# Kernel tuning notes

Hardware: AMD Instinct MI355X
Metric: run time of the kernel (lower is better)

The kernel has to match this reference:

```python
import jax, jax.numpy as jnp
import numpy as np

B, L, E, H = 4, 2048, 1024, 16
DK = E // H


def setup_inputs() -> dict:
    key = jax.random.key(0)
    k1, k2, k3 = jax.random.split(key, 3)
    x = jax.random.normal(k1, (B, L, E), dtype=jnp.float32)
    # torch Linear weights are [out, in]; xavier-ish scaling
    w_qkv = jax.random.normal(k2, (3 * E, E), dtype=jnp.float32) * (2.0 / (E + 3 * E)) ** 0.5
    wo = jax.random.normal(k3, (E, E), dtype=jnp.float32) * (1.0 / E) ** 0.5
    # causal mask: scores filled with -inf where mask == 0
    mask = jnp.tril(jnp.ones((L, L), dtype=bool))
    return {"x": x, "mask": mask, "w_qkv": w_qkv, "wo": wo}


def reference(x, mask, w_qkv, wo):
    b, l, e = x.shape
    # qkv projection: Linear with weight [3E, E] -> x @ W^T
    qkv = x @ w_qkv.T                              # [b, l, 3E]
    qkv = qkv.reshape(b, l, 3, H, DK)              # (three h d) split
    q = jnp.transpose(qkv[:, :, 0], (0, 2, 1, 3))  # [b, h, l, d]
    k = jnp.transpose(qkv[:, :, 1], (0, 2, 1, 3))
    v = jnp.transpose(qkv[:, :, 2], (0, 2, 1, 3))
    scores = jnp.einsum('bhld,bhmd->bhlm', q, k) / np.sqrt(DK)  # [b, h, l, l]
    scores = jnp.where(mask, scores, -jnp.inf)
    attn = jax.nn.softmax(scores, axis=-1)
    out = jnp.einsum('bhlm,bhmd->bhld', attn, v)   # [b, h, l, d]
    out = jnp.transpose(out, (0, 2, 1, 3)).reshape(b, l, e)  # b l (h d)
    return out @ wo.T
```

## Files before the change

kernel.cpp:

```cpp
#include <hip/hip_runtime.h>
#include <stdint.h>


typedef __bf16 bf16;
typedef __bf16 bf16x4 __attribute__((ext_vector_type(4)));
typedef __bf16 bf16x8 __attribute__((ext_vector_type(8)));
typedef float floatx4 __attribute__((ext_vector_type(4)));
typedef short s16x4 __attribute__((ext_vector_type(4)));

#define MFMA32(a, b, c) __builtin_amdgcn_mfma_f32_16x16x32_bf16(a, b, c, 0, 0, 0)
#define MFMA16(a, b, c) __builtin_amdgcn_mfma_f32_16x16x16bf16_1k(a, b, c, 0, 0, 0)

typedef const __attribute__((address_space(1))) uint32_t* gas_t;
typedef __attribute__((address_space(3))) uint32_t* las_t;

__device__ __forceinline__ void async16(void* lds, const void* g) {
  __builtin_amdgcn_global_load_lds((gas_t)g, (las_t)lds, 16, 0, 0);
}

__global__ void cvt_all(const float4* __restrict__ x, const float4* __restrict__ wq,
                        const float4* __restrict__ wo, bf16x4* __restrict__ xb,
                        bf16x4* __restrict__ wqb, bf16x4* __restrict__ wob) {
  const int NX = 2097152, NQ = 786432;
  int i = blockIdx.x * blockDim.x + threadIdx.x;
  float4 v;
  bf16x4* dst;
  int j;
  if (i < NX) { j = i; v = x[j]; dst = xb; }
  else if (i < NX + NQ) { j = i - NX; v = wq[j]; dst = wqb; }
  else { j = i - NX - NQ; v = wo[j]; dst = wob; }
  bf16x4 o;
  o[0] = (bf16)v.x; o[1] = (bf16)v.y; o[2] = (bf16)v.z; o[3] = (bf16)v.w;
  dst[j] = o;
}

__global__ __launch_bounds__(512, 2) void gemm_qkv(
    const bf16* __restrict__ A, const bf16* __restrict__ B,
    bf16* __restrict__ Qb, bf16* __restrict__ Kb, bf16* __restrict__ Vt) {
  __shared__ __align__(16) bf16 lds[2 * 24576];
  const int tid = threadIdx.x;
  const int wave = tid >> 6, lane = tid & 63;
  const int wr = wave >> 1, wc = wave & 1;
  const int l15 = lane & 15, quad = lane >> 4;

  const int bid = blockIdx.x;
  const int xcd = bid & 7, j = bid >> 3;
  const int mt_i = xcd * 4 + (j / 24);
  const int nt_i = j % 24;
  const int m0 = mt_i * 256, n0 = nt_i * 128;

  const int s_r = lane >> 3, s_c = lane & 7;

  auto unit = [&](bf16* dst, const bf16* src) {
#pragma unroll
    for (int i = 0; i < 2; ++i) {
      int g = wave * 2 + i;
      int row = g * 8 + s_r;
      async16(&dst[g * 512], src + (size_t)row * 1024 + ((s_c ^ (row & 7)) << 3));
    }
  };

  const bf16* Asrc = A + (size_t)m0 * 1024;
  const bf16* Bsrc = B + (size_t)n0 * 1024;

  auto rdA = [&](const bf16* cb, int mt, int kk) -> bf16x8 {
    int row = wr * 64 + mt * 16 + l15;
    return *(const bf16x8*)&cb[row * 64 + ((((kk << 2) | quad) ^ (l15 & 7)) << 3)];
  };
  auto rdB = [&](const bf16* cb, int nt, int kk) -> bf16x8 {
    int row = wc * 64 + nt * 16 + l15;
    return *(const bf16x8*)&cb[16384 + row * 64 +
                               ((((kk << 2) | quad) ^ (l15 & 7)) << 3)];
  };

  floatx4 acc[4][4] = {};

  unit(lds,         Asrc);
  unit(lds + 8192,  Asrc + (size_t)128 * 1024);
  unit(lds + 16384, Bsrc);

  auto body = [&](int t, bf16* cb, bf16* nb) {
    const int k1 = (t + 1) << 6;
    const bool pre = (t + 1) < 16;
    if (pre) {
      unit(nb, Asrc + k1);
      asm volatile("s_waitcnt vmcnt(2)" ::: "memory");
    } else {
      asm volatile("s_waitcnt vmcnt(0)" ::: "memory");
    }
    __builtin_amdgcn_s_barrier();
    asm volatile("" ::: "memory");
    bf16x8 bfr[4][2];
#pragma unroll
    for (int nt = 0; nt < 4; ++nt)
#pragma unroll
      for (int kk = 0; kk < 2; ++kk) bfr[nt][kk] = rdB(cb, nt, kk);
    bf16x8 af[2][2];
#pragma unroll
    for (int mt = 0; mt < 2; ++mt)
#pragma unroll
      for (int kk = 0; kk < 2; ++kk) af[mt][kk] = rdA(cb, mt, kk);
    __builtin_amdgcn_s_setprio(1);
#pragma unroll
    for (int mt = 0; mt < 2; ++mt)
#pragma unroll
      for (int nt = 0; nt < 4; ++nt)
#pragma unroll
        for (int kk = 0; kk < 2; ++kk)
          acc[mt][nt] = MFMA32(af[mt][kk], bfr[nt][kk], acc[mt][nt]);
    __builtin_amdgcn_s_setprio(0);
    if (pre) unit(nb + 8192, Asrc + (size_t)128 * 1024 + k1);
#pragma unroll
    for (int mt = 0; mt < 2; ++mt)
#pragma unroll
      for (int kk = 0; kk < 2; ++kk) af[mt][kk] = rdA(cb, mt + 2, kk);
    if (pre) unit(nb + 16384, Bsrc + k1);
    __builtin_amdgcn_s_setprio(1);
#pragma unroll
    for (int mt = 0; mt < 2; ++mt)
#pragma unroll
      for (int nt = 0; nt < 4; ++nt)
#pragma unroll
        for (int kk = 0; kk < 2; ++kk)
          acc[mt + 2][nt] = MFMA32(af[mt][kk], bfr[nt][kk], acc[mt + 2][nt]);
    __builtin_amdgcn_s_setprio(0);
    __builtin_amdgcn_s_barrier();
    asm volatile("" ::: "memory");
  };

  for (int tt = 0; tt < 8; ++tt) {
    body(2 * tt,     lds,         lds + 24576);
    body(2 * tt + 1, lds + 24576, lds);
  }

  if (n0 < 2048) {
    bf16* outp = (n0 < 1024) ? Qb : Kb;
    const int hd0 = n0 & 1023;
#pragma unroll
    for (int mt = 0; mt < 4; ++mt)
#pragma unroll
      for (int nt = 0; nt < 4; ++nt)
#pragma unroll
        for (int r = 0; r < 4; ++r) {
          int gm = m0 + wr * 64 + mt * 16 + quad * 4 + r;
          int gh = hd0 + wc * 64 + nt * 16 + l15;
          outp[(size_t)gm * 1024 + gh] = (bf16)acc[mt][nt][r];
        }
    return;
  }
  const int hd0 = n0 - 2048;
  const int bb = m0 >> 11, l_base = m0 & 2047;
#pragma unroll
  for (int mt = 0; mt < 4; ++mt)
#pragma unroll
    for (int nt = 0; nt < 4; ++nt) {
      int hd_l = wc * 64 + nt * 16 + l15;
      int l_l = wr * 64 + mt * 16 + quad * 4;
      bf16x4 tv;
#pragma unroll
      for (int r = 0; r < 4; ++r) tv[r] = (bf16)acc[mt][nt][r];
      *(bf16x4*)&lds[hd_l * 264 + l_l] = tv;
    }
  __syncthreads();
  const int rr = tid >> 5, cc = tid & 31;
#pragma unroll
  for (int it = 0; it < 8; ++it) {
    int row = it * 16 + rr;
    bf16x8 v = *(const bf16x8*)&lds[row * 264 + cc * 8];
    int hd = hd0 + row;
    *(bf16x8*)&Vt[((((size_t)bb * 16 + (hd >> 6)) * 64 + (hd & 63)) << 11) +
                  l_base + cc * 8] = v;
  }
}

__global__ __launch_bounds__(256) void gemm2_64(
    const bf16* __restrict__ A, const bf16* __restrict__ B,
    float* __restrict__ Cf, int M, int N, int K) {
  __shared__ __align__(16) bf16 As[64 * 32];
  __shared__ __align__(16) bf16 Bs[128 * 32];
  const int tid = threadIdx.x;
  const int wave = tid >> 6, lane = tid & 63;
  const int row0 = blockIdx.y * 64, col0 = blockIdx.x * 128;
  const int l15 = lane & 15, quad = lane >> 4;
  const int srow = lane >> 2, scol = (lane & 3) * 8;

  floatx4 acc[4][2] = {};

  for (int k0 = 0; k0 < K; k0 += 32) {
#pragma unroll
    for (int i = 0; i < 3; ++i) {
      int c = wave * 3 + i;
      if (c < 4)
        async16(&As[c * 512], A + (size_t)(row0 + c * 16 + srow) * K + k0 + scol);
      else
        async16(&Bs[(c - 4) * 512],
                B + (size_t)(col0 + (c - 4) * 16 + srow) * K + k0 + scol);
    }
    __syncthreads();
    bf16x8 af[4], bfr[2];
#pragma unroll
    for (int t = 0; t < 4; ++t)
      af[t] = *(const bf16x8*)&As[(t * 16 + l15) * 32 + quad * 8];
#pragma unroll
    for (int t = 0; t < 2; ++t)
      bfr[t] = *(const bf16x8*)&Bs[(wave * 32 + t * 16 + l15) * 32 + quad * 8];
#pragma unroll
    for (int mt = 0; mt < 4; ++mt)
#pragma unroll
      for (int nt = 0; nt < 2; ++nt)
        acc[mt][nt] = MFMA32(af[mt], bfr[nt], acc[mt][nt]);
    __syncthreads();
  }

#pragma unroll
  for (int mt = 0; mt < 4; ++mt)
#pragma unroll
    for (int nt = 0; nt < 2; ++nt)
#pragma unroll
      for (int r = 0; r < 4; ++r) {
        int gr = row0 + mt * 16 + quad * 4 + r;
        int gc = col0 + wave * 32 + nt * 16 + l15;
        Cf[(size_t)gr * N + gc] = acc[mt][nt][r];
      }
}

__global__ __launch_bounds__(256, 2) void flash_attn(
    const bf16* __restrict__ Qb, const bf16* __restrict__ Kb,
    const bf16* __restrict__ Vt, bf16* __restrict__ Ob) {
  const int bid0 = blockIdx.x;
  const int xcd = bid0 & 7, jj = bid0 >> 3;
  const int bh = xcd * 8 + (jj & 7);
  const int pr = jj >> 3;
  const int b = bh >> 4, h = bh & 15;
  const int tid = threadIdx.x;
  const int wave = tid >> 6, lane = tid & 63;
  const int l15 = lane & 15, quad = lane >> 4;

  const int qA = pr, qB = 31 - pr;

  __shared__ __align__(16) bf16 Ks2[2 * 64 * 64];
  __shared__ __align__(16) bf16 Vs2[2 * 64 * 64];

  const size_t x_base = (size_t)b * 2048 * 1024 + (size_t)h * 64;
  const size_t vt_base = (size_t)bh * 64 * 2048;

  const int k_lr = lane >> 3, k_c = lane & 7;

  auto stage = [&](int kt, int bufsel) {
    bf16* Kd = Ks2 + bufsel * 4096;
    bf16* Vd = Vs2 + bufsel * 4096;
#pragma unroll
    for (int i = 0; i < 2; ++i) {
      int o8 = wave * 2 + i;
      int row = o8 * 8 + k_lr;
      int sw = (k_c ^ (row & 7)) << 3;
      async16(&Kd[o8 * 512],
              Kb + x_base + (size_t)(kt * 64 + row) * 1024 + sw);
      async16(&Vd[o8 * 512],
              Vt + vt_base + (size_t)row * 2048 + kt * 64 + sw);
    }
  };

  auto load_q = [&](int q64, bf16x8* qf) {
#pragma unroll
    for (int ks = 0; ks < 2; ++ks) {
      const bf16* p = Qb + x_base +
          (size_t)(q64 * 64 + wave * 16 + l15) * 1024 + ks * 32 + quad * 8;
      bf16x8 v = *(const bf16x8*)p;
#pragma unroll
      for (int j = 0; j < 8; ++j) v[j] = (bf16)((float)v[j] * 0.18033688f);
      qf[ks] = v;
    }
  };

  stage(0, 0);

  bf16x8 qfA[2], qfB[2];
  load_q(qA, qfA);
  load_q(qB, qfB);

  floatx4 oA[4] = {}, oB[4] = {};
  float lA = 0.f, lB = 0.f;

  auto process = [&](const bf16x8* qf, floatx4* o, float& l_run,
                     int kt, int q64, bool diag, const bf16* Ks, const bf16* Vs) {
    floatx4 s[4] = {};
    __builtin_amdgcn_s_setprio(1);
#pragma unroll
    for (int nt = 0; nt < 4; ++nt) {
      int krow = nt * 16 + l15;
#pragma unroll
      for (int ks = 0; ks < 2; ++ks) {
        bf16x8 kf = *(const bf16x8*)&Ks[krow * 64 +
            ((((ks << 2) | quad) ^ (l15 & 7)) << 3)];
        s[nt] = MFMA32(kf, qf[ks], s[nt]);
      }
    }
    __builtin_amdgcn_s_setprio(0);
    if (diag) {
      int q_g = q64 * 64 + wave * 16 + l15;
#pragma unroll
      for (int nt = 0; nt < 4; ++nt)
#pragma unroll
        for (int r = 0; r < 4; ++r)
          if (kt * 64 + nt * 16 + quad * 4 + r > q_g) s[nt][r] = -__builtin_inff();
    }
    float ls = 0.f;
#pragma unroll
    for (int nt = 0; nt < 4; ++nt)
#pragma unroll
      for (int r = 0; r < 4; ++r) {
        float p = exp2f(s[nt][r]);
        s[nt][r] = p;
        ls += p;
      }
    l_run += ls;

    __builtin_amdgcn_s_setprio(1);
#pragma unroll
    for (int kb = 0; kb < 4; ++kb) {
      bf16x4 pb;
#pragma unroll
      for (int r = 0; r < 4; ++r) pb[r] = (bf16)s[kb][r];
      s16x4 pf = __builtin_bit_cast(s16x4, pb);
#pragma unroll
      for (int dt = 0; dt < 4; ++dt) {
        s16x4 vf = *(const s16x4*)&Vs[(dt * 16 + l15) * 64 +
            (((((kb << 1) | (quad >> 1)) ^ (l15 & 7))) << 3) + ((quad & 1) << 2)];
        o[dt] = MFMA16(vf, pf, o[dt]);
      }
    }
    __builtin_amdgcn_s_setprio(0);
  };

  __syncthreads();

  int cur = 0;
  for (int kt = 0; kt <= qB; ++kt) {
    if (kt < qB) stage(kt + 1, cur ^ 1);
    const bf16* Kc = Ks2 + cur * 4096;
    const bf16* Vc = Vs2 + cur * 4096;
    process(qfB, oB, lB, kt, qB, kt == qB, Kc, Vc);
    if (kt <= qA) process(qfA, oA, lA, kt, qA, kt == qA, Kc, Vc);
    __syncthreads();
    cur ^= 1;
  }

  auto store_o = [&](const floatx4* o, float l_run, int q64) {
    float lf = l_run;
    lf += __shfl_xor(lf, 16);
    lf += __shfl_xor(lf, 32);
    float inv = 1.0f / lf;
    size_t rowoff = x_base + (size_t)(q64 * 64 + wave * 16 + l15) * 1024;
#pragma unroll
    for (int dt = 0; dt < 4; ++dt) {
      bf16x4 ob;
#pragma unroll
      for (int r = 0; r < 4; ++r) ob[r] = (bf16)(o[dt][r] * inv);
      *(bf16x4*)(Ob + rowoff + dt * 16 + quad * 4) = ob;
    }
  };
  store_o(oA, lA, qA);
  store_o(oB, lB, qB);
}

extern "C" void kernel_launch(void* const* d_in, const int* in_sizes, int n_in,
                              void* d_out, int out_size, void* d_ws, size_t ws_size,
                              hipStream_t stream) {
  const float* x     = (const float*)d_in[0];
  const float* w_qkv = (const float*)d_in[2];
  const float* wo    = (const float*)d_in[3];
  float* out = (float*)d_out;

  char* ws = (char*)d_ws;
  bf16* xb  = (bf16*)(ws);
  bf16* wqb = (bf16*)(ws + (16u << 20));
  bf16* wob = (bf16*)(ws + (22u << 20));
  bf16* Qb  = (bf16*)(ws + (24u << 20));
  bf16* Kb  = (bf16*)(ws + (40u << 20));
  bf16* Vt  = (bf16*)(ws + (56u << 20));
  bf16* Ab  = (bf16*)(ws);

  cvt_all<<<12288, 256, 0, stream>>>((const float4*)x, (const float4*)w_qkv,
                                     (const float4*)wo, (bf16x4*)xb,
                                     (bf16x4*)wqb, (bf16x4*)wob);

  gemm_qkv<<<768, 512, 0, stream>>>(xb, wqb, Qb, Kb, Vt);
  flash_attn<<<1024, 256, 0, stream>>>(Qb, Kb, Vt, Ab);
  gemm2_64<<<dim3(8, 128), 256, 0, stream>>>(Ab, wob, out, 8192, 1024, 1024);
}
```

Baseline: 266.5 us.

## Double-buffer output projection GEMM with swizzled LDS and XCD-aware tile mapping

Rewrites the output-projection GEMM to double-buffer its LDS tiles, so the async global-to-LDS load for the next K slice overlaps the MFMAs on the current one, and it drops one barrier per iteration. An XOR swizzle on the 16-byte column chunks is meant to cut LDS bank conflicts on fragment reads. Blocks are remapped to a 1D grid so that neighbouring row tiles stay on the same XCD for L2 reuse, and wave priority is raised around the MFMAs. Dimensions are now hardcoded, so the kernel only handles this shape, and it uses twice the LDS.

Result: faster. 251.4 us (-5.7%).

```diff
diff --git a/kernel.cpp b/kernel.cpp
--- a/kernel.cpp
+++ b/kernel.cpp
@@ -175,41 +175,61 @@
 
 __global__ __launch_bounds__(256) void gemm2_64(
     const bf16* __restrict__ A, const bf16* __restrict__ B,
-    float* __restrict__ Cf, int M, int N, int K) {
-  __shared__ __align__(16) bf16 As[64 * 32];
-  __shared__ __align__(16) bf16 Bs[128 * 32];
+    float* __restrict__ Cf) {
+  __shared__ __align__(16) bf16 lds[2 * 6144];
   const int tid = threadIdx.x;
   const int wave = tid >> 6, lane = tid & 63;
-  const int row0 = blockIdx.y * 64, col0 = blockIdx.x * 128;
   const int l15 = lane & 15, quad = lane >> 4;
-  const int srow = lane >> 2, scol = (lane & 3) * 8;
-
-  floatx4 acc[4][2] = {};
-
-  for (int k0 = 0; k0 < K; k0 += 32) {
+  const int bid = blockIdx.x;
+  const int xcd = bid & 7, j = bid >> 3;
+  const int row0 = (xcd * 16 + (j >> 3)) * 64;
+  const int col0 = (j & 7) * 128;
+  const int s_r = lane >> 2, s_c = lane & 3;
+
+  auto stage = [&](int k0, bf16* buf) {
 #pragma unroll
     for (int i = 0; i < 3; ++i) {
       int c = wave * 3 + i;
-      if (c < 4)
-        async16(&As[c * 512], A + (size_t)(row0 + c * 16 + srow) * K + k0 + scol);
-      else
-        async16(&Bs[(c - 4) * 512],
-                B + (size_t)(col0 + (c - 4) * 16 + srow) * K + k0 + scol);
-    }
-    __syncthreads();
+      if (c < 4) {
+        int row = c * 16 + s_r;
+        async16(&buf[c * 512],
+                A + (size_t)(row0 + row) * 1024 + k0 + ((s_c ^ (row & 3)) << 3));
+      } else {
+        int row = (c - 4) * 16 + s_r;
+        async16(&buf[c * 512],
+                B + (size_t)(col0 + row) * 1024 + k0 + ((s_c ^ (row & 3)) << 3));
+      }
+    }
+  };
+
+  floatx4 acc[4][2] = {};
+  stage(0, lds);
+  __syncthreads();
+
+  int cur = 0;
+  for (int t = 0; t < 32; ++t) {
+    bf16* cb = lds + cur * 6144;
+    if (t < 31) stage((t + 1) << 5, lds + (cur ^ 1) * 6144);
     bf16x8 af[4], bfr[2];
 #pragma unroll
-    for (int t = 0; t < 4; ++t)
-      af[t] = *(const bf16x8*)&As[(t * 16 + l15) * 32 + quad * 8];
-#pragma unroll
-    for (int t = 0; t < 2; ++t)
-      bfr[t] = *(const bf16x8*)&Bs[(wave * 32 + t * 16 + l15) * 32 + quad * 8];
+    for (int mt = 0; mt < 4; ++mt) {
+      int row = mt * 16 + l15;
+      af[mt] = *(const bf16x8*)&cb[row * 32 + ((quad ^ (l15 & 3)) << 3)];
+    }
+#pragma unroll
+    for (int nt = 0; nt < 2; ++nt) {
+      int row = wave * 32 + nt * 16 + l15;
+      bfr[nt] = *(const bf16x8*)&cb[2048 + row * 32 + ((quad ^ (l15 & 3)) << 3)];
+    }
+    __builtin_amdgcn_s_setprio(1);
 #pragma unroll
     for (int mt = 0; mt < 4; ++mt)
 #pragma unroll
       for (int nt = 0; nt < 2; ++nt)
         acc[mt][nt] = MFMA32(af[mt], bfr[nt], acc[mt][nt]);
+    __builtin_amdgcn_s_setprio(0);
     __syncthreads();
+    cur ^= 1;
   }
 
 #pragma unroll
@@ -220,7 +240,7 @@
       for (int r = 0; r < 4; ++r) {
         int gr = row0 + mt * 16 + quad * 4 + r;
         int gc = col0 + wave * 32 + nt * 16 + l15;
-        Cf[(size_t)gr * N + gc] = acc[mt][nt][r];
+        Cf[(size_t)gr * 1024 + gc] = acc[mt][nt][r];
       }
 }
 
@@ -387,5 +407,5 @@
 
   gemm_qkv<<<768, 512, 0, stream>>>(xb, wqb, Qb, Kb, Vt);
   flash_attn<<<1024, 256, 0, stream>>>(Qb, Kb, Vt, Ab);
-  gemm2_64<<<dim3(8, 128), 256, 0, stream>>>(Ab, wob, out, 8192, 1024, 1024);
-}
+  gemm2_64<<<1024, 256, 0, stream>>>(Ab, wob, out);
+}
```

## Rewrite output projection GEMM with 256x128 tiles, double-buffered swizzled LDS

Applied to the files above, without the earlier changes.

Replaces the small 64x128 output-projection GEMM with a 512-thread kernel that computes 256x128 tiles using a BK=64 double-buffered LDS pipeline. Global-to-LDS loads for the next K step are interleaved with MFMA work, LDS uses an XOR swizzle to avoid bank conflicts, and blocks are remapped so tiles sharing rows stay on the same XCD. This aims to cut redundant global reads and hide memory latency in the final GEMM. In exchange it uses more LDS and registers per block, and the dimensions are hardcoded.

Measured after the change: 250.0 us. 6.2% less time.

```diff
diff --git a/kernel.cpp b/kernel.cpp
--- a/kernel.cpp
+++ b/kernel.cpp
@@ -173,54 +173,114 @@
   }
 }
 
-__global__ __launch_bounds__(256) void gemm2_64(
+__global__ __launch_bounds__(512, 2) void gemm2_256(
     const bf16* __restrict__ A, const bf16* __restrict__ B,
-    float* __restrict__ Cf, int M, int N, int K) {
-  __shared__ __align__(16) bf16 As[64 * 32];
-  __shared__ __align__(16) bf16 Bs[128 * 32];
+    float* __restrict__ Cf) {
+  __shared__ __align__(16) bf16 lds[2 * 24576];
   const int tid = threadIdx.x;
   const int wave = tid >> 6, lane = tid & 63;
-  const int row0 = blockIdx.y * 64, col0 = blockIdx.x * 128;
+  const int wr = wave >> 1, wc = wave & 1;
   const int l15 = lane & 15, quad = lane >> 4;
-  const int srow = lane >> 2, scol = (lane & 3) * 8;
-
-  floatx4 acc[4][2] = {};
-
-  for (int k0 = 0; k0 < K; k0 += 32) {
-#pragma unroll
-    for (int i = 0; i < 3; ++i) {
-      int c = wave * 3 + i;
-      if (c < 4)
-        async16(&As[c * 512], A + (size_t)(row0 + c * 16 + srow) * K + k0 + scol);
-      else
-        async16(&Bs[(c - 4) * 512],
-                B + (size_t)(col0 + (c - 4) * 16 + srow) * K + k0 + scol);
-    }
-    __syncthreads();
-    bf16x8 af[4], bfr[2];
-#pragma unroll
-    for (int t = 0; t < 4; ++t)
-      af[t] = *(const bf16x8*)&As[(t * 16 + l15) * 32 + quad * 8];
-#pragma unroll
-    for (int t = 0; t < 2; ++t)
-      bfr[t] = *(const bf16x8*)&Bs[(wave * 32 + t * 16 + l15) * 32 + quad * 8];
-#pragma unroll
-    for (int mt = 0; mt < 4; ++mt)
-#pragma unroll
-      for (int nt = 0; nt < 2; ++nt)
-        acc[mt][nt] = MFMA32(af[mt], bfr[nt], acc[mt][nt]);
-    __syncthreads();
+
+  const int bid = blockIdx.x;
+  const int xcd = bid & 7, j = bid >> 3;
+  const int mt_i = xcd * 4 + (j >> 3);
+  const int nt_i = j & 7;
+  const int m0 = mt_i * 256, n0 = nt_i * 128;
+
+  const int s_r = lane >> 3, s_c = lane & 7;
+
+  auto unit = [&](bf16* dst, const bf16* src) {
+#pragma unroll
+    for (int i = 0; i < 2; ++i) {
+      int g = wave * 2 + i;
+      int row = g * 8 + s_r;
+      async16(&dst[g * 512], src + (size_t)row * 1024 + ((s_c ^ (row & 7)) << 3));
+    }
+  };
+
+  const bf16* Asrc = A + (size_t)m0 * 1024;
+  const bf16* Bsrc = B + (size_t)n0 * 1024;
+
+  auto rdA = [&](const bf16* cb, int mt, int kk) -> bf16x8 {
+    int row = wr * 64 + mt * 16 + l15;
+    return *(const bf16x8*)&cb[row * 64 + ((((kk << 2) | quad) ^ (l15 & 7)) << 3)];
+  };
+  auto rdB = [&](const bf16* cb, int nt, int kk) -> bf16x8 {
+    int row = wc * 64 + nt * 16 + l15;
+    return *(const bf16x8*)&cb[16384 + row * 64 +
+                               ((((kk << 2) | quad) ^ (l15 & 7)) << 3)];
+  };
+
+  floatx4 acc[4][4] = {};
+
+  unit(lds,         Asrc);
+  unit(lds + 8192,  Asrc + (size_t)128 * 1024);
+  unit(lds + 16384, Bsrc);
+
+  auto body = [&](int t, bf16* cb, bf16* nb) {
+    const int k1 = (t + 1) << 6;
+    const bool pre = (t + 1) < 16;
+    if (pre) {
+      unit(nb, Asrc + k1);
+      asm volatile("s_waitcnt vmcnt(2)" ::: "memory");
+    } else {
+      asm volatile("s_waitcnt vmcnt(0)" ::: "memory");
+    }
+    __builtin_amdgcn_s_barrier();
+    asm volatile("" ::: "memory");
+    bf16x8 bfr[4][2];
+#pragma unroll
+    for (int nt = 0; nt < 4; ++nt)
+#pragma unroll
+      for (int kk = 0; kk < 2; ++kk) bfr[nt][kk] = rdB(cb, nt, kk);
+    bf16x8 af[2][2];
+#pragma unroll
+    for (int mt = 0; mt < 2; ++mt)
+#pragma unroll
+      for (int kk = 0; kk < 2; ++kk) af[mt][kk] = rdA(cb, mt, kk);
+    __builtin_amdgcn_s_setprio(1);
+#pragma unroll
+    for (int mt = 0; mt < 2; ++mt)
+#pragma unroll
+      for (int nt = 0; nt < 4; ++nt)
+#pragma unroll
+        for (int kk = 0; kk < 2; ++kk)
+          acc[mt][nt] = MFMA32(af[mt][kk], bfr[nt][kk], acc[mt][nt]);
+    __builtin_amdgcn_s_setprio(0);
+    if (pre) unit(nb + 8192, Asrc + (size_t)128 * 1024 + k1);
+#pragma unroll
+    for (int mt = 0; mt < 2; ++mt)
+#pragma unroll
+      for (int kk = 0; kk < 2; ++kk) af[mt][kk] = rdA(cb, mt + 2, kk);
+    if (pre) unit(nb + 16384, Bsrc + k1);
+    __builtin_amdgcn_s_setprio(1);
+#pragma unroll
+    for (int mt = 0; mt < 2; ++mt)
+#pragma unroll
+      for (int nt = 0; nt < 4; ++nt)
+#pragma unroll
+        for (int kk = 0; kk < 2; ++kk)
+          acc[mt + 2][nt] = MFMA32(af[mt][kk], bfr[nt][kk], acc[mt + 2][nt]);
+    __builtin_amdgcn_s_setprio(0);
+    __builtin_amdgcn_s_barrier();
+    asm volatile("" ::: "memory");
+  };
+
+  for (int tt = 0; tt < 8; ++tt) {
+    body(2 * tt,     lds,         lds + 24576);
+    body(2 * tt + 1, lds + 24576, lds);
   }
 
 #pragma unroll
   for (int mt = 0; mt < 4; ++mt)
 #pragma unroll
-    for (int nt = 0; nt < 2; ++nt)
+    for (int nt = 0; nt < 4; ++nt)
 #pragma unroll
       for (int r = 0; r < 4; ++r) {
-        int gr = row0 + mt * 16 + quad * 4 + r;
-        int gc = col0 + wave * 32 + nt * 16 + l15;
-        Cf[(size_t)gr * N + gc] = acc[mt][nt][r];
+        int gm = m0 + wr * 64 + mt * 16 + quad * 4 + r;
+        int gc = n0 + wc * 64 + nt * 16 + l15;
+        Cf[(size_t)gm * 1024 + gc] = acc[mt][nt][r];
       }
 }
 
@@ -387,5 +447,5 @@
 
   gemm_qkv<<<768, 512, 0, stream>>>(xb, wqb, Qb, Kb, Vt);
   flash_attn<<<1024, 256, 0, stream>>>(Qb, Kb, Vt, Ab);
-  gemm2_64<<<dim3(8, 128), 256, 0, stream>>>(Ab, wob, out, 8192, 1024, 1024);
-}
+  gemm2_256<<<256, 512, 0, stream>>>(Ab, wob, out);
+}
```
